# Performance work log

Measured on AMD Instinct MI355X. Metric: run time of the kernel, lower is better.

The kernel has to match this reference:

```python
import jax, jax.numpy as jnp
import numpy as np

VOCAB, E, H, B, T = 32000, 256, 256, 512, 128
PAD = 0
EPS = 1e-12


def setup_inputs() -> dict:
    key = jax.random.key(0)
    ks = jax.random.split(key, 20)
    captions = jax.random.randint(ks[0], (B, T), 0, VOCAB)
    emb = jax.random.normal(ks[1], (VOCAB, E), dtype=jnp.float32) * 0.02
    emb = emb.at[PAD].set(0.0)  # padding_idx row is zero in nn.Embedding
    s_in = 1.0 / np.sqrt(E)
    s_h = 1.0 / np.sqrt(H)
    d = {"captions": captions, "emb": emb}
    names = ["i", "f", "o", "c"]
    for j, n in enumerate(names):
        d[f"W_{n}"] = jax.random.uniform(ks[2 + 4 * j], (E, H), minval=-s_in, maxval=s_in)
        d[f"bW_{n}"] = jax.random.uniform(ks[3 + 4 * j], (H,), minval=-s_in, maxval=s_in)
        d[f"U_{n}"] = jax.random.uniform(ks[4 + 4 * j], (H, H), minval=-s_h, maxval=s_h)
        d[f"bU_{n}"] = jax.random.uniform(ks[5 + 4 * j], (H,), minval=-s_h, maxval=s_h)
    d["fc_w"] = jax.random.uniform(ks[18], (H, E), minval=-s_h, maxval=s_h)
    d["fc_b"] = jax.random.uniform(ks[19], (E,), minval=-s_h, maxval=s_h)
    return d


def _lstm_forward(captions, emb,
                  W_i, bW_i, U_i, bU_i,
                  W_f, bW_f, U_f, bU_f,
                  W_o, bW_o, U_o, bU_o,
                  W_c, bW_c, U_c, bU_c,
                  fc_w, fc_b):
    x = emb[captions]  # [B,T,E]
    mask = (captions != PAD).astype(x.dtype)[..., None]  # [B,T,1]
    # Precompute input-side gate projections for all timesteps (batched GEMM).
    xi = jnp.einsum("bte,eh->bth", x, W_i) + bW_i
    xf = jnp.einsum("bte,eh->bth", x, W_f) + bW_f
    xo = jnp.einsum("bte,eh->bth", x, W_o) + bW_o
    xg = jnp.einsum("bte,eh->bth", x, W_c) + bW_c
    # time-major for scan: [T,B,H]
    xs = (jnp.swapaxes(xi, 0, 1), jnp.swapaxes(xf, 0, 1),
          jnp.swapaxes(xo, 0, 1), jnp.swapaxes(xg, 0, 1),
          jnp.swapaxes(mask, 0, 1))
    h0 = jnp.zeros((captions.shape[0], U_i.shape[0]), dtype=x.dtype)
    c0 = jnp.zeros_like(h0)

    def step(carry, inp):
        h, c = carry
        xi_t, xf_t, xo_t, xg_t, m = inp
        g = jnp.tanh(xg_t + h @ U_c + bU_c)
        i = jax.nn.sigmoid(xi_t + h @ U_i + bU_i)
        f = jax.nn.sigmoid(xf_t + h @ U_f + bU_f)
        o = jax.nn.sigmoid(xo_t + h @ U_o + bU_o)
        c = i * g + f * c
        c = m * c + (1.0 - m) * jax.lax.stop_gradient(c)
        h = o * jnp.tanh(c)
        h = m * h + (1.0 - m) * jax.lax.stop_gradient(h)
        return (h, c), None

    (h, _), _ = jax.lax.scan(step, (h0, c0), xs)
    out = h @ fc_w + fc_b  # [B,E]
    norm = jnp.maximum(jnp.linalg.norm(out, axis=1, keepdims=True), EPS)
    return out / norm


def reference(captions, emb,
              W_i, bW_i, U_i, bU_i,
              W_f, bW_f, U_f, bU_f,
              W_o, bW_o, U_o, bU_o,
              W_c, bW_c, U_c, bU_c,
              fc_w, fc_b):
    return _lstm_forward(captions, emb,
                         W_i, bW_i, U_i, bU_i,
                         W_f, bW_f, U_f, bU_f,
                         W_o, bW_o, U_o, bU_o,
                         W_c, bW_c, U_c, bU_c,
                         fc_w, fc_b)
```

## Files before the change

### kernel.cpp

```cpp
#include <hip/hip_runtime.h>
#include <stdint.h>

typedef unsigned short ushort_t;
typedef __attribute__((ext_vector_type(8))) short bf8_t;
typedef __attribute__((ext_vector_type(4))) float f4_t;
typedef __attribute__((ext_vector_type(4))) unsigned short us4_t;

#define TT 128

__device__ __forceinline__ ushort_t f2bf(float f) {
  uint32_t u = __builtin_bit_cast(uint32_t, f);
  u += 0x7fffu + ((u >> 16) & 1u);
  return (ushort_t)(u >> 16);
}
__device__ __forceinline__ float bf2f(ushort_t h) {
  uint32_t u = ((uint32_t)h) << 16;
  return __builtin_bit_cast(float, u);
}
__device__ __forceinline__ float sigm(float x) {
  return __builtin_amdgcn_rcpf(1.f + __expf(-x));
}
__device__ __forceinline__ float tanh_f(float x) {
  return 1.f - 2.f * __builtin_amdgcn_rcpf(1.f + __expf(2.f * x));
}

__device__ __forceinline__ void store16_bypass(void* p, bf8_t v) {
  asm volatile("global_store_dwordx4 %0, %1, off sc0 sc1" :: "v"(p), "v"(v) : "memory");
}
__device__ __forceinline__ void store_flag_bypass(unsigned* p, unsigned v) {
  asm volatile("global_store_dword %0, %1, off sc0 sc1" :: "v"(p), "v"(v) : "memory");
}
__device__ __forceinline__ unsigned load_flag_bypass(const unsigned* p) {
  unsigned v;
  asm volatile("global_load_dword %0, %1, off sc0 sc1\n\ts_waitcnt vmcnt(0)"
               : "=v"(v) : "v"(p) : "memory");
  return v;
}
__device__ __forceinline__ void load4x16_bypass(const void* p, bf8_t f[4]) {
  asm volatile(
      "global_load_dwordx4 %0, %4, off sc0 sc1\n\t"
      "global_load_dwordx4 %1, %4, off offset:1024 sc0 sc1\n\t"
      "global_load_dwordx4 %2, %4, off offset:2048 sc0 sc1\n\t"
      "global_load_dwordx4 %3, %4, off offset:3072 sc0 sc1"
      : "=&v"(f[0]), "=&v"(f[1]), "=&v"(f[2]), "=&v"(f[3])
      : "v"(p) : "memory");
}

__global__ void k_pack_w(const float* W0, const float* W1, const float* W2, const float* W3,
                         ushort_t* __restrict__ o) {
  int idx = blockIdx.x * 256 + threadIdx.x;
  int n = idx >> 8, k = idx & 255;
  int g = n & 3, j = n >> 2;
  const float* Wg = g == 0 ? W0 : g == 1 ? W1 : g == 2 ? W2 : W3;
  o[(size_t)n * 256 + k] = f2bf(Wg[k * 256 + j]);
}

__global__ void k_pack_u(const float* U0, const float* U1, const float* U2, const float* U3,
                         ushort_t* __restrict__ o) {
  int idx = blockIdx.x * 256 + threadIdx.x;
  int lane = idx & 63, g = (idx >> 6) & 3, ktS = (idx >> 8) & 7,
      w = (idx >> 11) & 7, q = (idx >> 14) & 1;
  const float* Ug = g == 0 ? U0 : g == 1 ? U1 : g == 2 ? U2 : U3;
  int ktG = (ktS + 4 * q) & 7;
  int col = q * 128 + w * 16 + (lane & 15);
  int kb = ktG * 32 + (lane >> 4) * 8;
#pragma unroll
  for (int e = 0; e < 8; ++e)
    o[(size_t)idx * 8 + e] = f2bf(Ug[(size_t)(kb + e) * 256 + col]);
}

__global__ void k_bias(const float* a0, const float* a1, const float* a2, const float* a3,
                       const float* b0, const float* b1, const float* b2, const float* b3,
                       float* __restrict__ o) {
  int n = blockIdx.x * 256 + threadIdx.x;
  int g = n & 3, j = n >> 2;
  const float* pa = g == 0 ? a0 : g == 1 ? a1 : g == 2 ? a2 : a3;
  const float* pb = g == 0 ? b0 : g == 1 ? b1 : g == 2 ? b2 : b3;
  o[n] = pa[j] + pb[j];
}

__global__ __launch_bounds__(256) void k1_gemm(const float* __restrict__ A,
                                               const ushort_t* __restrict__ Bm,
                                               ushort_t* __restrict__ P) {
  __shared__ ushort_t Al[128 * 32];
  __shared__ ushort_t Bl[128 * 32];
  const int tid = threadIdx.x;
  const int lane = tid & 63;
  const int w = tid >> 6;
  const int mt = blockIdx.x >> 3;
  const int nt = blockIdx.x & 7;
  const int m0 = mt * 128, n0 = nt * 128;
  const int qr = (w >> 1) * 64, qc = (w & 1) * 64;

  f4_t acc[4][4];
#pragma unroll
  for (int i = 0; i < 4; ++i)
#pragma unroll
    for (int j = 0; j < 4; ++j) acc[i][j] = f4_t{0.f, 0.f, 0.f, 0.f};

  const int r0 = tid >> 2, s0 = tid & 3;
  const int r1 = 64 + r0;

  for (int k0 = 0; k0 < 256; k0 += 32) {
    float4 a00 = *(const float4*)(A + (size_t)(m0 + r0) * 256 + k0 + s0 * 8);
    float4 a01 = *(const float4*)(A + (size_t)(m0 + r0) * 256 + k0 + s0 * 8 + 4);
    float4 a10 = *(const float4*)(A + (size_t)(m0 + r1) * 256 + k0 + s0 * 8);
    float4 a11 = *(const float4*)(A + (size_t)(m0 + r1) * 256 + k0 + s0 * 8 + 4);
    bf8_t b0 = *(const bf8_t*)(Bm + (size_t)(n0 + r0) * 256 + k0 + s0 * 8);
    bf8_t b1 = *(const bf8_t*)(Bm + (size_t)(n0 + r1) * 256 + k0 + s0 * 8);
    bf8_t pa0, pa1;
    pa0[0] = (short)f2bf(a00.x); pa0[1] = (short)f2bf(a00.y);
    pa0[2] = (short)f2bf(a00.z); pa0[3] = (short)f2bf(a00.w);
    pa0[4] = (short)f2bf(a01.x); pa0[5] = (short)f2bf(a01.y);
    pa0[6] = (short)f2bf(a01.z); pa0[7] = (short)f2bf(a01.w);
    pa1[0] = (short)f2bf(a10.x); pa1[1] = (short)f2bf(a10.y);
    pa1[2] = (short)f2bf(a10.z); pa1[3] = (short)f2bf(a10.w);
    pa1[4] = (short)f2bf(a11.x); pa1[5] = (short)f2bf(a11.y);
    pa1[6] = (short)f2bf(a11.z); pa1[7] = (short)f2bf(a11.w);
    __syncthreads();
    *(bf8_t*)(Al + (size_t)tid * 8) = pa0;
    *(bf8_t*)(Al + (size_t)(256 + tid) * 8) = pa1;
    *(bf8_t*)(Bl + (size_t)tid * 8) = b0;
    *(bf8_t*)(Bl + (size_t)(256 + tid) * 8) = b1;
    __syncthreads();
    bf8_t af[4], bfr[4];
#pragma unroll
    for (int i = 0; i < 4; ++i) {
      af[i]  = *(const bf8_t*)(Al + (qr + i * 16 + (lane & 15)) * 32 + (lane >> 4) * 8);
      bfr[i] = *(const bf8_t*)(Bl + (qc + i * 16 + (lane & 15)) * 32 + (lane >> 4) * 8);
    }
#pragma unroll
    for (int i = 0; i < 4; ++i)
#pragma unroll
      for (int j = 0; j < 4; ++j)
        acc[i][j] = __builtin_amdgcn_mfma_f32_16x16x32_bf16(af[i], bfr[j], acc[i][j], 0, 0, 0);
  }
#pragma unroll
  for (int i = 0; i < 4; ++i)
#pragma unroll
    for (int j = 0; j < 4; ++j)
#pragma unroll
      for (int r = 0; r < 4; ++r) {
        int row = m0 + qr + i * 16 + (lane >> 4) * 4 + r;
        int col = n0 + qc + j * 16 + (lane & 15);
        P[(size_t)row * 1024 + col] = f2bf(acc[i][j][r]);
      }
}

__global__ __launch_bounds__(512, 2) void k_scan(
    const ushort_t* __restrict__ P, const ushort_t* __restrict__ UPJ,
    const float* __restrict__ bias, const int* __restrict__ cap,
    float* __restrict__ hfin, char* __restrict__ pbuf, unsigned* __restrict__ flags) {
  __shared__ ushort_t hlds[2][2048];
  const int blk = blockIdx.x;
  const int pair = blk >> 1, q = blk & 1;
  const int tid = threadIdx.x, lane = tid & 63, w = tid >> 6;
  const int l15 = lane & 15, l16 = lane >> 4;
  const int jc = q * 128 + w * 16 + l15;
  const int row0 = pair * 16 + l16 * 4;

  bf8_t u[8][4];
  {
    const ushort_t* ub = UPJ + (size_t)(q * 8 + w) * 32 * 512 + (size_t)lane * 8;
#pragma unroll
    for (int kt = 0; kt < 8; ++kt)
#pragma unroll
      for (int g = 0; g < 4; ++g)
        u[kt][g] = *(const bf8_t*)(ub + (kt * 4 + g) * 512);
  }
  const float4 bs = *(const float4*)(bias + jc * 4);

  float c[4] = {0.f, 0.f, 0.f, 0.f};
  f4_t acc[4];
#pragma unroll
  for (int g = 0; g < 4; ++g) acc[g] = f4_t{0.f, 0.f, 0.f, 0.f};

  us4_t pf[4];
#pragma unroll
  for (int r = 0; r < 4; ++r) {
    int tokr = cap[(row0 + r) * TT];
    pf[r] = *(const us4_t*)(P + (size_t)tokr * 1024 + jc * 4);
  }

  const int wfrag = (w >> 1) * 4 + (w & 1) * 2 + (l15 >> 3);
  const int wbase = wfrag * 128 + l16 * 32 + (l15 & 7);

  char* pairbuf = pbuf + (size_t)pair * 16384;
  unsigned* fown = flags + (pair * 2 + q) * TT;
  const unsigned* fpar = flags + (pair * 2 + (1 - q)) * TT;

  for (int t = 0; t < TT; ++t) {
    float hv[4];
#pragma unroll
    for (int r = 0; r < 4; ++r) {
      float pi = acc[0][r] + bf2f(pf[r].x) + bs.x;
      float pF = acc[1][r] + bf2f(pf[r].y) + bs.y;
      float po = acc[2][r] + bf2f(pf[r].z) + bs.z;
      float pg = acc[3][r] + bf2f(pf[r].w) + bs.w;
      float ig = sigm(pi), fg = sigm(pF), og = sigm(po), gg = tanh_f(pg);
      float cn = fmaf(fg, c[r], ig * gg);
      c[r] = cn;
      hv[r] = og * tanh_f(cn);
    }
    if (t == TT - 1) {
#pragma unroll
      for (int r = 0; r < 4; ++r)
        hfin[(size_t)(row0 + r) * 256 + jc] = hv[r];
      break;
    }
    const int par = t & 1;
    {
      ushort_t* hb = &hlds[par][0];
#pragma unroll
      for (int r = 0; r < 4; ++r) hb[wbase + r * 8] = f2bf(hv[r]);
    }
    __syncthreads();
    if (tid < 256) {
      bf8_t v = *(const bf8_t*)(&hlds[par][tid * 8]);
      store16_bypass(pairbuf + par * 8192 + q * 4096 + tid * 16, v);
    }
    asm volatile("s_waitcnt vmcnt(0)" ::: "memory");
    __syncthreads();
#pragma unroll
    for (int r = 0; r < 4; ++r) {
      int tokr = cap[(row0 + r) * TT + t + 1];
      pf[r] = *(const us4_t*)(P + (size_t)tokr * 1024 + jc * 4);
    }
    if (tid == 0) {
      store_flag_bypass(fown + t, 1u);
      while (load_flag_bypass(fpar + t) == 0) __builtin_amdgcn_s_sleep(1);
    }
    __syncthreads();
#pragma unroll
    for (int g = 0; g < 4; ++g) acc[g] = f4_t{0.f, 0.f, 0.f, 0.f};
    bf8_t paf[4];
    load4x16_bypass(pairbuf + par * 8192 + (1 - q) * 4096 + (l16 * 16 + l15) * 16, paf);
#pragma unroll
    for (int kt = 0; kt < 4; ++kt) {
      bf8_t afk = *(const bf8_t*)(&hlds[par][((kt * 4 + l16) * 16 + l15) * 8]);
#pragma unroll
      for (int g = 0; g < 4; ++g)
        acc[g] = __builtin_amdgcn_mfma_f32_16x16x32_bf16(afk, u[kt][g], acc[g], 0, 0, 0);
    }
    asm volatile("s_waitcnt vmcnt(0)" ::: "memory");
    __builtin_amdgcn_sched_barrier(0);
#pragma unroll
    for (int kt = 0; kt < 4; ++kt)
#pragma unroll
      for (int g = 0; g < 4; ++g)
        acc[g] = __builtin_amdgcn_mfma_f32_16x16x32_bf16(paf[kt], u[4 + kt][g], acc[g], 0, 0, 0);
  }
}

__global__ __launch_bounds__(256) void k3_fc(const float* __restrict__ hfin,
                                             const float* __restrict__ fcw,
                                             const float* __restrict__ fcb,
                                             float* __restrict__ out) {
  __shared__ float hrow[256];
  __shared__ float red[4];
  const int b = blockIdx.x, j = threadIdx.x;
  hrow[j] = hfin[(size_t)b * 256 + j];
  __syncthreads();
  float acc = fcb[j];
#pragma unroll 4
  for (int k = 0; k < 256; ++k) acc = fmaf(hrow[k], fcw[(size_t)k * 256 + j], acc);
  float ss = acc * acc;
#pragma unroll
  for (int o = 32; o > 0; o >>= 1) ss += __shfl_down(ss, o);
  if ((j & 63) == 0) red[j >> 6] = ss;
  __syncthreads();
  float tot = red[0] + red[1] + red[2] + red[3];
  float nrm = fmaxf(sqrtf(tot), 1e-12f);
  out[(size_t)b * 256 + j] = acc / nrm;
}

extern "C" void kernel_launch(void* const* d_in, const int* in_sizes, int n_in,
                              void* d_out, int out_size, void* d_ws, size_t ws_size,
                              hipStream_t stream) {
  const int* captions = (const int*)d_in[0];
  const float* emb = (const float*)d_in[1];
  const float *W[4], *bW[4], *U[4], *bU[4];
  for (int g = 0; g < 4; ++g) {
    W[g]  = (const float*)d_in[2 + 4 * g];
    bW[g] = (const float*)d_in[3 + 4 * g];
    U[g]  = (const float*)d_in[4 + 4 * g];
    bU[g] = (const float*)d_in[5 + 4 * g];
  }
  const float* fcw = (const float*)d_in[18];
  const float* fcb = (const float*)d_in[19];
  float* out = (float*)d_out;

  char* ws = (char*)d_ws;
  ushort_t* P     = (ushort_t*)(ws);
  ushort_t* WT    = (ushort_t*)(ws + 65536000);
  ushort_t* UPJ   = (ushort_t*)(ws + 66060288);
  float*    bias  = (float*)   (ws + 66584576);
  float*    hfin  = (float*)   (ws + 66588672);
  char*     pbuf  = (char*)    (ws + 67112960);
  unsigned* flags = (unsigned*)(ws + 67637248);

  hipMemsetAsync(flags, 0, 32768, stream);
  k_pack_w<<<1024, 256, 0, stream>>>(W[0], W[1], W[2], W[3], WT);
  k_pack_u<<<128, 256, 0, stream>>>(U[0], U[1], U[2], U[3], UPJ);
  k_bias<<<4, 256, 0, stream>>>(bW[0], bW[1], bW[2], bW[3],
                                bU[0], bU[1], bU[2], bU[3], bias);
  k1_gemm<<<2000, 256, 0, stream>>>(emb, WT, P);
  k_scan<<<64, 512, 0, stream>>>(P, UPJ, bias, captions, hfin, pbuf, flags);
  k3_fc<<<512, 256, 0, stream>>>(hfin, fcw, fcb, out);
}
```

Baseline: 444.6 us.

## Process two 16-row batch groups per scan block and prefetch tokens ahead

The LSTM scan kernel now handles 32 batch rows per block pair (two independent 16-row groups A and B) instead of 16, halving the grid from 64 to 32 blocks. Both groups share the register-resident U weights, and their exchange and flag handshakes are issued together, so one group's MFMAs can overlap the other's cross-block wait. Token indices are prefetched two steps ahead and the P gate rows one step ahead, so those dependent loads leave the serial critical path. The cost is fewer blocks in flight and roughly twice the per-step work and registers in each block.

```diff
diff --git a/kernel.cpp b/kernel.cpp
--- a/kernel.cpp
+++ b/kernel.cpp
@@ -24,26 +24,19 @@
   return 1.f - 2.f * __builtin_amdgcn_rcpf(1.f + __expf(2.f * x));
 }
 
-__device__ __forceinline__ void store16_bypass(void* p, bf8_t v) {
+__device__ __forceinline__ void x_store16(void* p, bf8_t v) {
   asm volatile("global_store_dwordx4 %0, %1, off sc0 sc1" :: "v"(p), "v"(v) : "memory");
 }
-__device__ __forceinline__ void store_flag_bypass(unsigned* p, unsigned v) {
+__device__ __forceinline__ void x_store_flag(unsigned* p, unsigned v) {
   asm volatile("global_store_dword %0, %1, off sc0 sc1" :: "v"(p), "v"(v) : "memory");
 }
-__device__ __forceinline__ unsigned load_flag_bypass(const unsigned* p) {
-  unsigned v;
-  asm volatile("global_load_dword %0, %1, off sc0 sc1\n\ts_waitcnt vmcnt(0)"
-               : "=v"(v) : "v"(p) : "memory");
-  return v;
-}
-__device__ __forceinline__ void load4x16_bypass(const void* p, bf8_t f[4]) {
+__device__ __forceinline__ void x_load4_issue(const void* p, bf8_t f[4]) {
   asm volatile(
       "global_load_dwordx4 %0, %4, off sc0 sc1\n\t"
       "global_load_dwordx4 %1, %4, off offset:1024 sc0 sc1\n\t"
       "global_load_dwordx4 %2, %4, off offset:2048 sc0 sc1\n\t"
       "global_load_dwordx4 %3, %4, off offset:3072 sc0 sc1"
-      : "=&v"(f[0]), "=&v"(f[1]), "=&v"(f[2]), "=&v"(f[3])
-      : "v"(p) : "memory");
+      : "=&v"(f[0]), "=&v"(f[1]), "=&v"(f[2]), "=&v"(f[3]) : "v"(p) : "memory");
 }
 
 __global__ void k_pack_w(const float* W0, const float* W1, const float* W2, const float* W3,
@@ -147,17 +140,19 @@
       }
 }
 
+#define OFFX(pp, G, par, qq) ((((((pp) * 2 + (G)) * 2 + (par)) * 2) + (qq)) * 4096)
 __global__ __launch_bounds__(512, 2) void k_scan(
     const ushort_t* __restrict__ P, const ushort_t* __restrict__ UPJ,
     const float* __restrict__ bias, const int* __restrict__ cap,
     float* __restrict__ hfin, char* __restrict__ pbuf, unsigned* __restrict__ flags) {
-  __shared__ ushort_t hlds[2][2048];
+  __shared__ ushort_t hlds[2][2][2048];
   const int blk = blockIdx.x;
   const int pair = blk >> 1, q = blk & 1;
   const int tid = threadIdx.x, lane = tid & 63, w = tid >> 6;
   const int l15 = lane & 15, l16 = lane >> 4;
   const int jc = q * 128 + w * 16 + l15;
-  const int row0 = pair * 16 + l16 * 4;
+  const int rowA = pair * 32 + l16 * 4;
+  const int rowB = rowA + 16;
 
   bf8_t u[8][4];
   {
@@ -170,86 +165,139 @@
   }
   const float4 bs = *(const float4*)(bias + jc * 4);
 
-  float c[4] = {0.f, 0.f, 0.f, 0.f};
-  f4_t acc[4];
-#pragma unroll
-  for (int g = 0; g < 4; ++g) acc[g] = f4_t{0.f, 0.f, 0.f, 0.f};
-
-  us4_t pf[4];
+  float cA[4] = {0.f, 0.f, 0.f, 0.f}, cB[4] = {0.f, 0.f, 0.f, 0.f};
+  f4_t accA[4], accB[4];
+#pragma unroll
+  for (int g = 0; g < 4; ++g) { accA[g] = f4_t{0.f,0.f,0.f,0.f}; accB[g] = f4_t{0.f,0.f,0.f,0.f}; }
+
+  int tokA[4], tokB[4];
+  us4_t pfA[4], pfB[4];
+#pragma unroll
+  for (int r = 0; r < 4; ++r) { tokA[r] = cap[(rowA + r) * TT]; tokB[r] = cap[(rowB + r) * TT]; }
 #pragma unroll
   for (int r = 0; r < 4; ++r) {
-    int tokr = cap[(row0 + r) * TT];
-    pf[r] = *(const us4_t*)(P + (size_t)tokr * 1024 + jc * 4);
-  }
+    pfA[r] = *(const us4_t*)(P + (size_t)tokA[r] * 1024 + jc * 4);
+    pfB[r] = *(const us4_t*)(P + (size_t)tokB[r] * 1024 + jc * 4);
+  }
+#pragma unroll
+  for (int r = 0; r < 4; ++r) { tokA[r] = cap[(rowA + r) * TT + 1]; tokB[r] = cap[(rowB + r) * TT + 1]; }
 
   const int wfrag = (w >> 1) * 4 + (w & 1) * 2 + (l15 >> 3);
   const int wbase = wfrag * 128 + l16 * 32 + (l15 & 7);
-
-  char* pairbuf = pbuf + (size_t)pair * 16384;
-  unsigned* fown = flags + (pair * 2 + q) * TT;
-  const unsigned* fpar = flags + (pair * 2 + (1 - q)) * TT;
+  const int cg = tid >> 8, ct = tid & 255;
+
+  unsigned* fownA = flags + ((pair * 2 + q) * 2 + 0) * TT;
+  unsigned* fownB = flags + ((pair * 2 + q) * 2 + 1) * TT;
+  const unsigned* fparA = flags + ((pair * 2 + (1 - q)) * 2 + 0) * TT;
+  const unsigned* fparB = flags + ((pair * 2 + (1 - q)) * 2 + 1) * TT;
+
+#define GATES(cX, pfX, accX, hvX)                                        \
+  _Pragma("unroll")                                                      \
+  for (int r = 0; r < 4; ++r) {                                          \
+    float pi = accX[0][r] + bf2f(pfX[r].x) + bs.x;                       \
+    float pF = accX[1][r] + bf2f(pfX[r].y) + bs.y;                       \
+    float po = accX[2][r] + bf2f(pfX[r].z) + bs.z;                       \
+    float pg = accX[3][r] + bf2f(pfX[r].w) + bs.w;                       \
+    float ig = sigm(pi), fg = sigm(pF), og = sigm(po), gg = tanh_f(pg);  \
+    float cn = fmaf(fg, cX[r], ig * gg);                                 \
+    cX[r] = cn;                                                          \
+    hvX[r] = og * tanh_f(cn);                                            \
+  }
 
   for (int t = 0; t < TT; ++t) {
-    float hv[4];
+    float hvA[4], hvB[4];
+    GATES(cA, pfA, accA, hvA)
+    GATES(cB, pfB, accB, hvB)
+    if (t == TT - 1) {
+#pragma unroll
+      for (int r = 0; r < 4; ++r) {
+        hfin[(size_t)(rowA + r) * 256 + jc] = hvA[r];
+        hfin[(size_t)(rowB + r) * 256 + jc] = hvB[r];
+      }
+      break;
+    }
+    const int par = t & 1;
 #pragma unroll
     for (int r = 0; r < 4; ++r) {
-      float pi = acc[0][r] + bf2f(pf[r].x) + bs.x;
-      float pF = acc[1][r] + bf2f(pf[r].y) + bs.y;
-      float po = acc[2][r] + bf2f(pf[r].z) + bs.z;
-      float pg = acc[3][r] + bf2f(pf[r].w) + bs.w;
-      float ig = sigm(pi), fg = sigm(pF), og = sigm(po), gg = tanh_f(pg);
-      float cn = fmaf(fg, c[r], ig * gg);
-      c[r] = cn;
-      hv[r] = og * tanh_f(cn);
-    }
-    if (t == TT - 1) {
-#pragma unroll
-      for (int r = 0; r < 4; ++r)
-        hfin[(size_t)(row0 + r) * 256 + jc] = hv[r];
-      break;
-    }
-    const int par = t & 1;
+      hlds[0][par][wbase + r * 8] = f2bf(hvA[r]);
+      hlds[1][par][wbase + r * 8] = f2bf(hvB[r]);
+    }
+    __syncthreads();
     {
-      ushort_t* hb = &hlds[par][0];
-#pragma unroll
-      for (int r = 0; r < 4; ++r) hb[wbase + r * 8] = f2bf(hv[r]);
+      bf8_t v = *(const bf8_t*)(&hlds[cg][par][ct * 8]);
+      x_store16(pbuf + OFFX(pair, cg, par, q) + ct * 16, v);
+      asm volatile("s_waitcnt vmcnt(0)" ::: "memory");
     }
     __syncthreads();
-    if (tid < 256) {
-      bf8_t v = *(const bf8_t*)(&hlds[par][tid * 8]);
-      store16_bypass(pairbuf + par * 8192 + q * 4096 + tid * 16, v);
-    }
-    asm volatile("s_waitcnt vmcnt(0)" ::: "memory");
-    __syncthreads();
-#pragma unroll
-    for (int r = 0; r < 4; ++r) {
-      int tokr = cap[(row0 + r) * TT + t + 1];
-      pf[r] = *(const us4_t*)(P + (size_t)tokr * 1024 + jc * 4);
-    }
-    if (tid == 0) {
-      store_flag_bypass(fown + t, 1u);
-      while (load_flag_bypass(fpar + t) == 0) __builtin_amdgcn_s_sleep(1);
-    }
-    __syncthreads();
-#pragma unroll
-    for (int g = 0; g < 4; ++g) acc[g] = f4_t{0.f, 0.f, 0.f, 0.f};
-    bf8_t paf[4];
-    load4x16_bypass(pairbuf + par * 8192 + (1 - q) * 4096 + (l16 * 16 + l15) * 16, paf);
+    if (tid == 0)   x_store_flag(fownA + t, 1u);
+    if (tid == 256) x_store_flag(fownB + t, 1u);
+    us4_t pfnA[4], pfnB[4];
+    int tokNA[4], tokNB[4];
+    {
+      const int t2 = (t + 2 < TT) ? t + 2 : TT - 1;
+#pragma unroll
+      for (int r = 0; r < 4; ++r) {
+        pfnA[r] = *(const us4_t*)(P + (size_t)tokA[r] * 1024 + jc * 4);
+        pfnB[r] = *(const us4_t*)(P + (size_t)tokB[r] * 1024 + jc * 4);
+      }
+#pragma unroll
+      for (int r = 0; r < 4; ++r) {
+        tokNA[r] = cap[(rowA + r) * TT + t2];
+        tokNB[r] = cap[(rowB + r) * TT + t2];
+      }
+    }
+    {
+      unsigned fa, fb;
+      for (;;) {
+        asm volatile(
+            "global_load_dword %0, %2, off sc0 sc1\n\t"
+            "global_load_dword %1, %3, off sc0 sc1\n\t"
+            "s_waitcnt vmcnt(0)"
+            : "=&v"(fa), "=&v"(fb) : "v"(fparA + t), "v"(fparB + t) : "memory");
+        if ((fa & fb) != 0u) break;
+        __builtin_amdgcn_s_sleep(1);
+      }
+    }
+    bf8_t pafA[4], pafB[4];
+    x_load4_issue(pbuf + OFFX(pair, 0, par, 1 - q) + (l16 * 16 + l15) * 16, pafA);
+    x_load4_issue(pbuf + OFFX(pair, 1, par, 1 - q) + (l16 * 16 + l15) * 16, pafB);
+#pragma unroll
+    for (int g = 0; g < 4; ++g) { accA[g] = f4_t{0.f,0.f,0.f,0.f}; accB[g] = f4_t{0.f,0.f,0.f,0.f}; }
 #pragma unroll
     for (int kt = 0; kt < 4; ++kt) {
-      bf8_t afk = *(const bf8_t*)(&hlds[par][((kt * 4 + l16) * 16 + l15) * 8]);
-#pragma unroll
-      for (int g = 0; g < 4; ++g)
-        acc[g] = __builtin_amdgcn_mfma_f32_16x16x32_bf16(afk, u[kt][g], acc[g], 0, 0, 0);
-    }
+      bf8_t afk = *(const bf8_t*)(&hlds[0][par][((kt * 4 + l16) * 16 + l15) * 8]);
+#pragma unroll
+      for (int g = 0; g < 4; ++g)
+        accA[g] = __builtin_amdgcn_mfma_f32_16x16x32_bf16(afk, u[kt][g], accA[g], 0, 0, 0);
+    }
+#pragma unroll
+    for (int kt = 0; kt < 4; ++kt) {
+      bf8_t bfk = *(const bf8_t*)(&hlds[1][par][((kt * 4 + l16) * 16 + l15) * 8]);
+#pragma unroll
+      for (int g = 0; g < 4; ++g)
+        accB[g] = __builtin_amdgcn_mfma_f32_16x16x32_bf16(bfk, u[kt][g], accB[g], 0, 0, 0);
+    }
+    asm volatile("s_waitcnt vmcnt(4)" ::: "memory");
+    __builtin_amdgcn_sched_barrier(0);
+#pragma unroll
+    for (int kt = 0; kt < 4; ++kt)
+#pragma unroll
+      for (int g = 0; g < 4; ++g)
+        accA[g] = __builtin_amdgcn_mfma_f32_16x16x32_bf16(pafA[kt], u[4 + kt][g], accA[g], 0, 0, 0);
     asm volatile("s_waitcnt vmcnt(0)" ::: "memory");
     __builtin_amdgcn_sched_barrier(0);
 #pragma unroll
     for (int kt = 0; kt < 4; ++kt)
 #pragma unroll
       for (int g = 0; g < 4; ++g)
-        acc[g] = __builtin_amdgcn_mfma_f32_16x16x32_bf16(paf[kt], u[4 + kt][g], acc[g], 0, 0, 0);
-  }
+        accB[g] = __builtin_amdgcn_mfma_f32_16x16x32_bf16(pafB[kt], u[4 + kt][g], accB[g], 0, 0, 0);
+#pragma unroll
+    for (int r = 0; r < 4; ++r) {
+      pfA[r] = pfnA[r]; pfB[r] = pfnB[r];
+      tokA[r] = tokNA[r]; tokB[r] = tokNB[r];
+    }
+  }
+#undef GATES
 }
 
 __global__ __launch_bounds__(256) void k3_fc(const float* __restrict__ hfin,
@@ -305,6 +353,6 @@
   k_bias<<<4, 256, 0, stream>>>(bW[0], bW[1], bW[2], bW[3],
                                 bU[0], bU[1], bU[2], bU[3], bias);
   k1_gemm<<<2000, 256, 0, stream>>>(emb, WT, P);
-  k_scan<<<64, 512, 0, stream>>>(P, UPJ, bias, captions, hfin, pbuf, flags);
+  k_scan<<<32, 512, 0, stream>>>(P, UPJ, bias, captions, hfin, pbuf, flags);
   k3_fc<<<512, 256, 0, stream>>>(hfin, fcw, fcb, out);
 }
```

After: 1.290 ms. 2.9x slower.

## Gather tokens inside the input GEMM and replace scan barriers with per-wave flags

Applied to the files above, without the earlier changes.

The input-projection GEMM now gathers embedding rows per (batch, time) token and folds in the combined bias. This produces a per-step gate table that the scan reads sequentially instead of gathering from a per-vocab table. In the recurrent loop, the two block-wide barriers and single-thread flag polling are replaced by per-wave byte flags that all threads poll. The next-step gate prefetch is moved after the partner-h load so it overlaps with the MFMAs, using a partial vmcnt wait. The trade-off is a GEMM over twice as many rows and a doubled workspace, in exchange for a shorter serial critical path per timestep.

```diff
diff --git a/kernel.cpp b/kernel.cpp
--- a/kernel.cpp
+++ b/kernel.cpp
@@ -24,26 +24,25 @@
   return 1.f - 2.f * __builtin_amdgcn_rcpf(1.f + __expf(2.f * x));
 }
 
-__device__ __forceinline__ void store16_bypass(void* p, bf8_t v) {
+__device__ __forceinline__ void x_store16(void* p, bf8_t v) {
   asm volatile("global_store_dwordx4 %0, %1, off sc0 sc1" :: "v"(p), "v"(v) : "memory");
 }
-__device__ __forceinline__ void store_flag_bypass(unsigned* p, unsigned v) {
-  asm volatile("global_store_dword %0, %1, off sc0 sc1" :: "v"(p), "v"(v) : "memory");
-}
-__device__ __forceinline__ unsigned load_flag_bypass(const unsigned* p) {
+__device__ __forceinline__ void x_store_flag_byte(void* p, unsigned v) {
+  asm volatile("global_store_byte %0, %1, off sc0 sc1" :: "v"(p), "v"(v) : "memory");
+}
+__device__ __forceinline__ unsigned x_load_flag(const void* p) {
   unsigned v;
   asm volatile("global_load_dword %0, %1, off sc0 sc1\n\ts_waitcnt vmcnt(0)"
                : "=v"(v) : "v"(p) : "memory");
   return v;
 }
-__device__ __forceinline__ void load4x16_bypass(const void* p, bf8_t f[4]) {
+__device__ __forceinline__ void x_load4_issue(const void* p, bf8_t f[4]) {
   asm volatile(
       "global_load_dwordx4 %0, %4, off sc0 sc1\n\t"
       "global_load_dwordx4 %1, %4, off offset:1024 sc0 sc1\n\t"
       "global_load_dwordx4 %2, %4, off offset:2048 sc0 sc1\n\t"
       "global_load_dwordx4 %3, %4, off offset:3072 sc0 sc1"
-      : "=&v"(f[0]), "=&v"(f[1]), "=&v"(f[2]), "=&v"(f[3])
-      : "v"(p) : "memory");
+      : "=&v"(f[0]), "=&v"(f[1]), "=&v"(f[2]), "=&v"(f[3]) : "v"(p) : "memory");
 }
 
 __global__ void k_pack_w(const float* W0, const float* W1, const float* W2, const float* W3,
@@ -55,8 +54,8 @@
   o[(size_t)n * 256 + k] = f2bf(Wg[k * 256 + j]);
 }
 
-__global__ void k_pack_u(const float* U0, const float* U1, const float* U2, const float* U3,
-                         ushort_t* __restrict__ o) {
+__global__ void k_pack_u2(const float* U0, const float* U1, const float* U2, const float* U3,
+                          ushort_t* __restrict__ o) {
   int idx = blockIdx.x * 256 + threadIdx.x;
   int lane = idx & 63, g = (idx >> 6) & 3, ktS = (idx >> 8) & 7,
       w = (idx >> 11) & 7, q = (idx >> 14) & 1;
@@ -79,9 +78,11 @@
   o[n] = pa[j] + pb[j];
 }
 
-__global__ __launch_bounds__(256) void k1_gemm(const float* __restrict__ A,
-                                               const ushort_t* __restrict__ Bm,
-                                               ushort_t* __restrict__ P) {
+__global__ __launch_bounds__(256) void k1g_gemm(const float* __restrict__ A,
+                                                const ushort_t* __restrict__ Bm,
+                                                const float* __restrict__ bias,
+                                                const int* __restrict__ cap,
+                                                ushort_t* __restrict__ Pg) {
   __shared__ ushort_t Al[128 * 32];
   __shared__ ushort_t Bl[128 * 32];
   const int tid = threadIdx.x;
@@ -100,12 +101,14 @@
 
   const int r0 = tid >> 2, s0 = tid & 3;
   const int r1 = 64 + r0;
+  const int t0 = cap[m0 + r0];
+  const int t1 = cap[m0 + r1];
 
   for (int k0 = 0; k0 < 256; k0 += 32) {
-    float4 a00 = *(const float4*)(A + (size_t)(m0 + r0) * 256 + k0 + s0 * 8);
-    float4 a01 = *(const float4*)(A + (size_t)(m0 + r0) * 256 + k0 + s0 * 8 + 4);
-    float4 a10 = *(const float4*)(A + (size_t)(m0 + r1) * 256 + k0 + s0 * 8);
-    float4 a11 = *(const float4*)(A + (size_t)(m0 + r1) * 256 + k0 + s0 * 8 + 4);
+    float4 a00 = *(const float4*)(A + (size_t)t0 * 256 + k0 + s0 * 8);
+    float4 a01 = *(const float4*)(A + (size_t)t0 * 256 + k0 + s0 * 8 + 4);
+    float4 a10 = *(const float4*)(A + (size_t)t1 * 256 + k0 + s0 * 8);
+    float4 a11 = *(const float4*)(A + (size_t)t1 * 256 + k0 + s0 * 8 + 4);
     bf8_t b0 = *(const bf8_t*)(Bm + (size_t)(n0 + r0) * 256 + k0 + s0 * 8);
     bf8_t b1 = *(const bf8_t*)(Bm + (size_t)(n0 + r1) * 256 + k0 + s0 * 8);
     bf8_t pa0, pa1;
@@ -143,14 +146,13 @@
       for (int r = 0; r < 4; ++r) {
         int row = m0 + qr + i * 16 + (lane >> 4) * 4 + r;
         int col = n0 + qc + j * 16 + (lane & 15);
-        P[(size_t)row * 1024 + col] = f2bf(acc[i][j][r]);
+        Pg[(size_t)row * 1024 + col] = f2bf(acc[i][j][r] + bias[col]);
       }
 }
 
-__global__ __launch_bounds__(512, 2) void k_scan(
-    const ushort_t* __restrict__ P, const ushort_t* __restrict__ UPJ,
-    const float* __restrict__ bias, const int* __restrict__ cap,
-    float* __restrict__ hfin, char* __restrict__ pbuf, unsigned* __restrict__ flags) {
+__global__ __launch_bounds__(512, 2) void k_scan4(
+    const ushort_t* __restrict__ Pg, const ushort_t* __restrict__ UPJ,
+    float* __restrict__ hfin, char* __restrict__ pbuf, char* __restrict__ flags) {
   __shared__ ushort_t hlds[2][2048];
   const int blk = blockIdx.x;
   const int pair = blk >> 1, q = blk & 1;
@@ -168,7 +170,11 @@
       for (int g = 0; g < 4; ++g)
         u[kt][g] = *(const bf8_t*)(ub + (kt * 4 + g) * 512);
   }
-  const float4 bs = *(const float4*)(bias + jc * 4);
+
+  const ushort_t* pg[4];
+#pragma unroll
+  for (int r = 0; r < 4; ++r)
+    pg[r] = Pg + ((size_t)(row0 + r) * TT) * 1024 + jc * 4;
 
   float c[4] = {0.f, 0.f, 0.f, 0.f};
   f4_t acc[4];
@@ -177,27 +183,23 @@
 
   us4_t pf[4];
 #pragma unroll
-  for (int r = 0; r < 4; ++r) {
-    int tokr = cap[(row0 + r) * TT];
-    pf[r] = *(const us4_t*)(P + (size_t)tokr * 1024 + jc * 4);
-  }
+  for (int r = 0; r < 4; ++r) { pf[r] = *(const us4_t*)pg[r]; pg[r] += 1024; }
 
   const int wfrag = (w >> 1) * 4 + (w & 1) * 2 + (l15 >> 3);
   const int wbase = wfrag * 128 + l16 * 32 + (l15 & 7);
-
   char* pairbuf = pbuf + (size_t)pair * 16384;
-  unsigned* fown = flags + (pair * 2 + q) * TT;
-  const unsigned* fpar = flags + (pair * 2 + (1 - q)) * TT;
+  char* fown = flags + (size_t)(pair * 2 + q) * TT * 4;
+  const char* fpar = flags + (size_t)(pair * 2 + (1 - q)) * TT * 4;
 
   for (int t = 0; t < TT; ++t) {
     float hv[4];
 #pragma unroll
     for (int r = 0; r < 4; ++r) {
-      float pi = acc[0][r] + bf2f(pf[r].x) + bs.x;
-      float pF = acc[1][r] + bf2f(pf[r].y) + bs.y;
-      float po = acc[2][r] + bf2f(pf[r].z) + bs.z;
-      float pg = acc[3][r] + bf2f(pf[r].w) + bs.w;
-      float ig = sigm(pi), fg = sigm(pF), og = sigm(po), gg = tanh_f(pg);
+      float pi = acc[0][r] + bf2f(pf[r].x);
+      float pF = acc[1][r] + bf2f(pf[r].y);
+      float po = acc[2][r] + bf2f(pf[r].z);
+      float pg_ = acc[3][r] + bf2f(pf[r].w);
+      float ig = sigm(pi), fg = sigm(pF), og = sigm(po), gg = tanh_f(pg_);
       float cn = fmaf(fg, c[r], ig * gg);
       c[r] = cn;
       hv[r] = og * tanh_f(cn);
@@ -217,24 +219,23 @@
     __syncthreads();
     if (tid < 256) {
       bf8_t v = *(const bf8_t*)(&hlds[par][tid * 8]);
-      store16_bypass(pairbuf + par * 8192 + q * 4096 + tid * 16, v);
-    }
-    asm volatile("s_waitcnt vmcnt(0)" ::: "memory");
-    __syncthreads();
-#pragma unroll
-    for (int r = 0; r < 4; ++r) {
-      int tokr = cap[(row0 + r) * TT + t + 1];
-      pf[r] = *(const us4_t*)(P + (size_t)tokr * 1024 + jc * 4);
-    }
-    if (tid == 0) {
-      store_flag_bypass(fown + t, 1u);
-      while (load_flag_bypass(fpar + t) == 0) __builtin_amdgcn_s_sleep(1);
-    }
-    __syncthreads();
+      x_store16(pairbuf + par * 8192 + q * 4096 + tid * 16, v);
+      asm volatile("s_waitcnt vmcnt(0)" ::: "memory");
+      if (lane == 0) x_store_flag_byte(fown + t * 4 + w, 1u);
+    }
+    {
+      unsigned fv = x_load_flag(fpar + t * 4);
+      while (fv != 0x01010101u) {
+        __builtin_amdgcn_s_sleep(1);
+        fv = x_load_flag(fpar + t * 4);
+      }
+    }
 #pragma unroll
     for (int g = 0; g < 4; ++g) acc[g] = f4_t{0.f, 0.f, 0.f, 0.f};
     bf8_t paf[4];
-    load4x16_bypass(pairbuf + par * 8192 + (1 - q) * 4096 + (l16 * 16 + l15) * 16, paf);
+    x_load4_issue(pairbuf + par * 8192 + (1 - q) * 4096 + (l16 * 16 + l15) * 16, paf);
+#pragma unroll
+    for (int r = 0; r < 4; ++r) { pf[r] = *(const us4_t*)pg[r]; pg[r] += 1024; }
 #pragma unroll
     for (int kt = 0; kt < 4; ++kt) {
       bf8_t afk = *(const bf8_t*)(&hlds[par][((kt * 4 + l16) * 16 + l15) * 8]);
@@ -242,7 +243,7 @@
       for (int g = 0; g < 4; ++g)
         acc[g] = __builtin_amdgcn_mfma_f32_16x16x32_bf16(afk, u[kt][g], acc[g], 0, 0, 0);
     }
-    asm volatile("s_waitcnt vmcnt(0)" ::: "memory");
+    asm volatile("s_waitcnt vmcnt(4)" ::: "memory");
     __builtin_amdgcn_sched_barrier(0);
 #pragma unroll
     for (int kt = 0; kt < 4; ++kt)
@@ -289,22 +290,22 @@
   const float* fcw = (const float*)d_in[18];
   const float* fcb = (const float*)d_in[19];
   float* out = (float*)d_out;
-
   char* ws = (char*)d_ws;
-  ushort_t* P     = (ushort_t*)(ws);
-  ushort_t* WT    = (ushort_t*)(ws + 65536000);
-  ushort_t* UPJ   = (ushort_t*)(ws + 66060288);
-  float*    bias  = (float*)   (ws + 66584576);
-  float*    hfin  = (float*)   (ws + 66588672);
-  char*     pbuf  = (char*)    (ws + 67112960);
-  unsigned* flags = (unsigned*)(ws + 67637248);
+
+  ushort_t* Pg    = (ushort_t*)(ws);
+  ushort_t* WT    = (ushort_t*)(ws + 134217728);
+  ushort_t* UPJ2  = (ushort_t*)(ws + 134742016);
+  float*    bias  = (float*)   (ws + 135266304);
+  float*    hfin  = (float*)   (ws + 135270400);
+  char*     pbuf  = (char*)    (ws + 135794688);
+  char*     flags = (char*)    (ws + 136318976);
 
   hipMemsetAsync(flags, 0, 32768, stream);
   k_pack_w<<<1024, 256, 0, stream>>>(W[0], W[1], W[2], W[3], WT);
-  k_pack_u<<<128, 256, 0, stream>>>(U[0], U[1], U[2], U[3], UPJ);
+  k_pack_u2<<<128, 256, 0, stream>>>(U[0], U[1], U[2], U[3], UPJ2);
   k_bias<<<4, 256, 0, stream>>>(bW[0], bW[1], bW[2], bW[3],
                                 bU[0], bU[1], bU[2], bU[3], bias);
-  k1_gemm<<<2000, 256, 0, stream>>>(emb, WT, P);
-  k_scan<<<64, 512, 0, stream>>>(P, UPJ, bias, captions, hfin, pbuf, flags);
+  k1g_gemm<<<4096, 256, 0, stream>>>(emb, WT, bias, captions, Pg);
+  k_scan4<<<64, 512, 0, stream>>>(Pg, UPJ2, hfin, pbuf, flags);
   k3_fc<<<512, 256, 0, stream>>>(hfin, fcw, fcb, out);
 }
```

After: 441.4 us. No clear change (-0.7%).
